# Kernel tuning notes

Measured on AMD Instinct MI355X. Metric: run time of the kernel, lower is better.

Reference implementation:

```python
import jax, jax.numpy as jnp
import numpy as np

STDS = np.array([0.1, 0.1, 0.2, 0.2], np.float32)
MEANS = np.array([0.0, 0.0, 0.0, 0.0], np.float32)
NMS_THRESH = 0.3  # cfg.TEST.NMS


def _decode_clip(boxes, deltas, iminfo):
    # boxes [R,4] (x1,y1,x2,y2), deltas [R,C,4] (unnormalized), iminfo [3]=(h,w,scale)
    w = boxes[:, 2] - boxes[:, 0] + 1.0
    h = boxes[:, 3] - boxes[:, 1] + 1.0
    cx = boxes[:, 0] + 0.5 * w
    cy = boxes[:, 1] + 0.5 * h
    pcx = deltas[..., 0] * w[:, None] + cx[:, None]
    pcy = deltas[..., 1] * h[:, None] + cy[:, None]
    pw = jnp.exp(deltas[..., 2]) * w[:, None]
    ph = jnp.exp(deltas[..., 3]) * h[:, None]
    x1 = pcx - 0.5 * pw
    y1 = pcy - 0.5 * ph
    x2 = pcx + 0.5 * pw
    y2 = pcy + 0.5 * ph
    x1 = jnp.clip(x1, 0.0, iminfo[1] - 1.0)
    x2 = jnp.clip(x2, 0.0, iminfo[1] - 1.0)
    y1 = jnp.clip(y1, 0.0, iminfo[0] - 1.0)
    y2 = jnp.clip(y2, 0.0, iminfo[0] - 1.0)
    return jnp.stack([x1, y1, x2, y2], axis=-1)  # [R,C,4]


def _nms_keep(boxes, valid):
    # boxes [R,4] sorted by score desc; valid [R] bool. Greedy hard NMS, fixed shape.
    b = jax.lax.stop_gradient(boxes)
    R = b.shape[0]
    x1, y1, x2, y2 = b[:, 0], b[:, 1], b[:, 2], b[:, 3]
    area = jnp.maximum(x2 - x1, 0.0) * jnp.maximum(y2 - y1, 0.0)
    xx1 = jnp.maximum(x1[:, None], x1[None, :])
    yy1 = jnp.maximum(y1[:, None], y1[None, :])
    xx2 = jnp.minimum(x2[:, None], x2[None, :])
    yy2 = jnp.minimum(y2[:, None], y2[None, :])
    inter = jnp.maximum(xx2 - xx1, 0.0) * jnp.maximum(yy2 - yy1, 0.0)
    iou = inter / (area[:, None] + area[None, :] - inter + 1e-9)
    ar = jnp.arange(R)
    def body(i, keep):
        sup = (iou[i] > NMS_THRESH) & (ar > i) & keep[i]
        return keep & ~sup
    return jax.lax.fori_loop(0, R, body, valid)


def _per_class(scores, boxes, thresh, cls_id):
    # scores [R], boxes [R,4], scalar thresh, scalar class id
    valid = scores > thresh
    s = jnp.where(valid, scores, -jnp.inf)
    order = jnp.argsort(-s)
    b = boxes[order]
    v = valid[order]
    keep = _nms_keep(b, v)
    dets = jnp.concatenate([b, jnp.full((b.shape[0], 1), cls_id, b.dtype)], axis=1)  # [R,5]
    return dets, keep


def _per_image(scores, pred_boxes, thr, num_pad):
    # scores [R,C], pred_boxes [R,C,4], thr [C]
    C = scores.shape[1]
    cls_ids = jnp.arange(1, C, dtype=scores.dtype)
    dets, keep = jax.vmap(_per_class, in_axes=(1, 1, 0, 0))(
        scores[:, 1:], pred_boxes[:, 1:], thr[1:], cls_ids)  # [C-1,R,5], [C-1,R]
    dets = dets.reshape(-1, 5)   # class-major order == torch.cat over classes
    keep = keep.reshape(-1)
    pos = jnp.cumsum(keep) - 1
    write = keep & (pos < num_pad)  # truncate to num_pad like the original
    idx = jnp.where(write, pos, num_pad)  # overflow bucket
    out = jnp.zeros((num_pad + 1, 5), dets.dtype).at[idx].add(
        dets * write[:, None].astype(dets.dtype))
    n = jnp.minimum(keep.sum(), num_pad)
    return out[:num_pad], n  # zero-padded [num_pad,5], count


def reference(cls_prob, rois, bbox_pred, im_info, per_class_threshold, num_classes):
    B, R, C = cls_prob.shape
    deltas = bbox_pred.reshape(B, R, C, 4) * STDS + MEANS
    pred = jax.vmap(_decode_clip)(rois[:, :, 1:5], deltas, im_info)  # [B,R,C,4]
    gt, n = jax.vmap(lambda s, p: _per_image(s, p, per_class_threshold, num_classes))(
        cls_prob, pred)
    return gt, n


def setup_inputs() -> dict:
    key = jax.random.key(0)
    B, R, C = 2, 1000, 81
    ks = jax.random.split(key, 6)
    cls_prob = jax.nn.softmax(2.0 * jax.random.normal(ks[0], (B, R, C)), axis=-1)
    cx = jax.random.uniform(ks[1], (B, R)) * 1200.0 + 50.0
    cy = jax.random.uniform(ks[2], (B, R)) * 700.0 + 50.0
    bw = jax.random.uniform(ks[3], (B, R)) * 300.0 + 16.0
    bh = jax.random.uniform(ks[4], (B, R)) * 300.0 + 16.0
    x1 = jnp.clip(cx - 0.5 * bw, 0.0, 1332.0)
    x2 = jnp.clip(cx + 0.5 * bw, 0.0, 1332.0)
    y1 = jnp.clip(cy - 0.5 * bh, 0.0, 799.0)
    y2 = jnp.clip(cy + 0.5 * bh, 0.0, 799.0)
    rois = jnp.concatenate([jnp.zeros((B, R, 1)), jnp.stack([x1, y1, x2, y2], -1)], -1)
    bbox_pred = 0.5 * jax.random.normal(ks[5], (B, R, 4 * C))
    im_info = jnp.tile(jnp.array([[800.0, 1333.0, 1.0]], jnp.float32), (B, 1))
    per_class_threshold = jnp.full((C,), 0.05, jnp.float32)
    return {"cls_prob": cls_prob, "rois": rois, "bbox_pred": bbox_pred,
            "im_info": im_info, "per_class_threshold": per_class_threshold,
            "num_classes": C}
```

## Files before the change

### kernel.cpp

```cpp
#include <hip/hip_runtime.h>
#include <math.h>

#define MAXC 1024
#define NMS_T 0.3f

__global__ __launch_bounds__(256) void nms_class_kernel(
    const float* __restrict__ cls_prob, const float* __restrict__ rois,
    const float* __restrict__ bbox_pred, const float* __restrict__ im_info,
    const float* __restrict__ thr, float* __restrict__ ws_boxes,
    int* __restrict__ ws_counts, int B, int R, int C)
{
    const int task = blockIdx.x;
    const int NC = C - 1;
    const int b = task / NC;
    const int c = 1 + (task % NC);
    const int tid = threadIdx.x;

    __shared__ int s_cnt;
    __shared__ float s_sc[MAXC];
    __shared__ int   s_ri[MAXC];
    __shared__ float s_bx[MAXC][4];
    __shared__ float s_area[MAXC];
    __shared__ int   s_keep[MAXC];

    if (tid == 0) s_cnt = 0;
    __syncthreads();

    const float tc = thr[c];
    for (int r = tid; r < R; r += blockDim.x) {
        float s = cls_prob[((size_t)b * R + r) * C + c];
        if (s > tc) {
            int p = atomicAdd(&s_cnt, 1);
            if (p < MAXC) { s_sc[p] = s; s_ri[p] = r; }
        }
    }
    __syncthreads();
    int K = s_cnt; if (K > MAXC) K = MAXC;

    const float maxx = im_info[b * 3 + 1] - 1.0f;
    const float maxy = im_info[b * 3 + 0] - 1.0f;

    for (int i = tid; i < K; i += blockDim.x) {
        const float si = s_sc[i];
        const int   ri = s_ri[i];
        int rank = 0;
        for (int j = 0; j < K; j++) {
            float sj = s_sc[j];
            rank += (sj > si) || (sj == si && s_ri[j] < ri);
        }
        const float* rp = rois + ((size_t)b * R + ri) * 5;
        float rx1 = rp[1], ry1 = rp[2], rx2 = rp[3], ry2 = rp[4];
        float w  = rx2 - rx1 + 1.0f;
        float h  = ry2 - ry1 + 1.0f;
        float cx = rx1 + 0.5f * w;
        float cy = ry1 + 0.5f * h;
        const float* dp = bbox_pred + (((size_t)b * R + ri) * C + c) * 4;
        float d0 = dp[0] * 0.1f, d1 = dp[1] * 0.1f;
        float d2 = dp[2] * 0.2f, d3 = dp[3] * 0.2f;
        float pcx = d0 * w + cx;
        float pcy = d1 * h + cy;
        float pw  = expf(d2) * w;
        float ph  = expf(d3) * h;
        float x1 = fminf(fmaxf(pcx - 0.5f * pw, 0.0f), maxx);
        float x2 = fminf(fmaxf(pcx + 0.5f * pw, 0.0f), maxx);
        float y1 = fminf(fmaxf(pcy - 0.5f * ph, 0.0f), maxy);
        float y2 = fminf(fmaxf(pcy + 0.5f * ph, 0.0f), maxy);
        s_bx[rank][0] = x1; s_bx[rank][1] = y1;
        s_bx[rank][2] = x2; s_bx[rank][3] = y2;
        s_area[rank] = fmaxf(x2 - x1, 0.0f) * fmaxf(y2 - y1, 0.0f);
        s_keep[rank] = 1;
    }
    __syncthreads();

    for (int i = 0; i < K; i++) {
        __syncthreads();
        if (s_keep[i]) {
            float bx1 = s_bx[i][0], by1 = s_bx[i][1];
            float bx2 = s_bx[i][2], by2 = s_bx[i][3];
            float ai  = s_area[i];
            for (int j = i + 1 + tid; j < K; j += blockDim.x) {
                if (s_keep[j]) {
                    float xx1 = fmaxf(bx1, s_bx[j][0]);
                    float yy1 = fmaxf(by1, s_bx[j][1]);
                    float xx2 = fminf(bx2, s_bx[j][2]);
                    float yy2 = fminf(by2, s_bx[j][3]);
                    float inter = fmaxf(xx2 - xx1, 0.0f) * fmaxf(yy2 - yy1, 0.0f);
                    float iou = inter / (ai + s_area[j] - inter + 1e-9f);
                    if (iou > NMS_T) s_keep[j] = 0;
                }
            }
        }
    }
    __syncthreads();

    if (tid == 0) {
        float* dst = ws_boxes + (size_t)task * C * 5;
        int kept = 0;
        float cid = (float)c;
        for (int i = 0; i < K; i++) {
            if (s_keep[i]) {
                if (kept < C) {
                    dst[kept * 5 + 0] = s_bx[i][0];
                    dst[kept * 5 + 1] = s_bx[i][1];
                    dst[kept * 5 + 2] = s_bx[i][2];
                    dst[kept * 5 + 3] = s_bx[i][3];
                    dst[kept * 5 + 4] = cid;
                }
                kept++;
            }
        }
        ws_counts[task] = kept;
    }
}

__global__ __launch_bounds__(256) void pack_kernel(
    const float* __restrict__ ws_boxes, const int* __restrict__ ws_counts,
    float* __restrict__ gt, float* __restrict__ nout, int B, int C)
{
    const int b = blockIdx.x;
    const int tid = threadIdx.x;
    const int NC = C - 1;
    const int P = C;
    __shared__ int s_off[256];
    __shared__ int s_total;

    if (tid == 0) {
        int acc = 0;
        for (int c = 0; c < NC; c++) { s_off[c] = acc; acc += ws_counts[b * NC + c]; }
        s_total = acc;
    }
    __syncthreads();
    const int n = (s_total < P) ? s_total : P;

    for (int i = tid; i < P * 5; i += blockDim.x)
        gt[(size_t)b * P * 5 + i] = 0.0f;
    __syncthreads();

    for (int idx = tid; idx < NC * P; idx += blockDim.x) {
        int c = idx / P, k = idx % P;
        int cnt = ws_counts[b * NC + c]; if (cnt > P) cnt = P;
        if (k < cnt) {
            int pos = s_off[c] + k;
            if (pos < P) {
                const float* src = ws_boxes + (((size_t)(b * NC + c)) * P + k) * 5;
                float* d = gt + ((size_t)b * P + pos) * 5;
                d[0] = src[0]; d[1] = src[1]; d[2] = src[2]; d[3] = src[3]; d[4] = src[4];
            }
        }
    }
    if (tid == 0) nout[b] = (float)n;
}

extern "C" void kernel_launch(void* const* d_in, const int* in_sizes, int n_in,
                              void* d_out, int out_size, void* d_ws, size_t ws_size,
                              hipStream_t stream) {
    const float* cls_prob  = (const float*)d_in[0];
    const float* rois      = (const float*)d_in[1];
    const float* bbox_pred = (const float*)d_in[2];
    const float* im_info   = (const float*)d_in[3];
    const float* thr       = (const float*)d_in[4];

    const int B = in_sizes[3] / 3;
    const int C = in_sizes[4];
    const int R = in_sizes[0] / (B * C);
    const int NC = C - 1;

    float* ws_boxes = (float*)d_ws;
    int*   ws_counts = (int*)(ws_boxes + (size_t)B * NC * C * 5);

    float* gt   = (float*)d_out;
    float* nout = (float*)d_out + (size_t)B * C * 5;

    nms_class_kernel<<<B * NC, 256, 0, stream>>>(
        cls_prob, rois, bbox_pred, im_info, thr, ws_boxes, ws_counts, B, R, C);
    pack_kernel<<<B, 256, 0, stream>>>(ws_boxes, ws_counts, gt, nout, B, C);
}
```

Baseline: 100.5 us.

## Run per-class NMS in a single wavefront with ballot-based compaction and register keep masks

Shrinks the NMS block to one 64-lane wavefront. Candidate compaction now uses ballot and popcount instead of shared atomics. When there are at most 256 candidates, greedy suppression runs on register-resident boxes with 64-bit keep masks updated by ballot, which removes the per-iteration __syncthreads. Kept boxes are written in parallel instead of by a single thread. The pack kernel also computes its prefix offsets in parallel from cached counts. The trade-off is fewer threads per block for the rank and decode phase, plus a slower fallback path when there are more than 256 candidates.

```diff
diff --git a/kernel.cpp b/kernel.cpp
--- a/kernel.cpp
+++ b/kernel.cpp
@@ -4,7 +4,7 @@
 #define MAXC 1024
 #define NMS_T 0.3f
 
-__global__ __launch_bounds__(256) void nms_class_kernel(
+__global__ __launch_bounds__(64) void nms_class_kernel(
     const float* __restrict__ cls_prob, const float* __restrict__ rois,
     const float* __restrict__ bbox_pred, const float* __restrict__ im_info,
     const float* __restrict__ thr, float* __restrict__ ws_boxes,
@@ -15,38 +15,48 @@
     const int b = task / NC;
     const int c = 1 + (task % NC);
     const int tid = threadIdx.x;
-
-    __shared__ int s_cnt;
-    __shared__ float s_sc[MAXC];
-    __shared__ int   s_ri[MAXC];
-    __shared__ float s_bx[MAXC][4];
-    __shared__ float s_area[MAXC];
-    __shared__ int   s_keep[MAXC];
-
-    if (tid == 0) s_cnt = 0;
-    __syncthreads();
+    const unsigned long long lane_lt = (1ull << tid) - 1ull;
+
+    __shared__ float  s_sc[MAXC];
+    __shared__ int    s_ri[MAXC];
+    __shared__ float4 s_bx[MAXC];
+    __shared__ float  s_area[MAXC];
+    __shared__ int    s_keep[MAXC];
 
     const float tc = thr[c];
-    for (int r = tid; r < R; r += blockDim.x) {
-        float s = cls_prob[((size_t)b * R + r) * C + c];
-        if (s > tc) {
-            int p = atomicAdd(&s_cnt, 1);
-            if (p < MAXC) { s_sc[p] = s; s_ri[p] = r; }
-        }
-    }
-    __syncthreads();
-    int K = s_cnt; if (K > MAXC) K = MAXC;
+    int base = 0;
+    for (int r0 = 0; r0 < R; r0 += 64 * 16) {
+        float v[16];
+#pragma unroll
+        for (int k = 0; k < 16; k++) {
+            int r = r0 + k * 64 + tid;
+            v[k] = (r < R) ? cls_prob[((size_t)b * R + r) * C + c] : -1.0f;
+        }
+#pragma unroll
+        for (int k = 0; k < 16; k++) {
+            int r = r0 + k * 64 + tid;
+            bool valid = v[k] > tc;
+            unsigned long long m = __ballot(valid);
+            if (valid) {
+                int pos = base + __popcll(m & lane_lt);
+                if (pos < MAXC) { s_sc[pos] = v[k]; s_ri[pos] = r; }
+            }
+            base += __popcll(m);
+        }
+    }
+    int K = (base < MAXC) ? base : MAXC;
+    __syncthreads();
 
     const float maxx = im_info[b * 3 + 1] - 1.0f;
     const float maxy = im_info[b * 3 + 0] - 1.0f;
 
-    for (int i = tid; i < K; i += blockDim.x) {
-        const float si = s_sc[i];
-        const int   ri = s_ri[i];
+    for (int cand = tid; cand < K; cand += 64) {
+        const float si = s_sc[cand];
+        const int   ri = s_ri[cand];
         int rank = 0;
         for (int j = 0; j < K; j++) {
-            float sj = s_sc[j];
-            rank += (sj > si) || (sj == si && s_ri[j] < ri);
+            float sj = s_sc[j]; int rj = s_ri[j];
+            rank += (sj > si) || (sj == si && rj < ri);
         }
         const float* rp = rois + ((size_t)b * R + ri) * 5;
         float rx1 = rp[1], ry1 = rp[2], rx2 = rp[3], ry2 = rp[4];
@@ -65,51 +75,107 @@
         float x2 = fminf(fmaxf(pcx + 0.5f * pw, 0.0f), maxx);
         float y1 = fminf(fmaxf(pcy - 0.5f * ph, 0.0f), maxy);
         float y2 = fminf(fmaxf(pcy + 0.5f * ph, 0.0f), maxy);
-        s_bx[rank][0] = x1; s_bx[rank][1] = y1;
-        s_bx[rank][2] = x2; s_bx[rank][3] = y2;
+        s_bx[rank] = make_float4(x1, y1, x2, y2);
         s_area[rank] = fmaxf(x2 - x1, 0.0f) * fmaxf(y2 - y1, 0.0f);
-        s_keep[rank] = 1;
-    }
-    __syncthreads();
-
-    for (int i = 0; i < K; i++) {
+    }
+    __syncthreads();
+
+    float* dst = ws_boxes + (size_t)task * C * 5;
+    const float cid = (float)c;
+    const int nchunk = (K + 63) >> 6;
+
+    if (nchunk <= 4) {
+        float jx1[4], jy1[4], jx2[4], jy2[4], jar[4];
+        unsigned long long km[4];
+#pragma unroll
+        for (int q = 0; q < 4; q++) {
+            int idx = q * 64 + tid;
+            float4 bj = (idx < K) ? s_bx[idx] : make_float4(0.f, 0.f, 0.f, 0.f);
+            jx1[q] = bj.x; jy1[q] = bj.y; jx2[q] = bj.z; jy2[q] = bj.w;
+            jar[q] = (idx < K) ? s_area[idx] : 0.0f;
+            int rem = K - q * 64;
+            km[q] = (rem >= 64) ? ~0ull : ((rem > 0) ? ((1ull << rem) - 1ull) : 0ull);
+        }
+        for (int i = 0; i < K; i++) {
+            int ci = i >> 6, li = i & 63;
+            unsigned long long kw = (ci == 0) ? km[0] : (ci == 1) ? km[1]
+                                   : (ci == 2) ? km[2] : km[3];
+            if ((kw >> li) & 1ull) {
+                float4 bi = s_bx[i];
+                float ai = s_area[i];
+#pragma unroll
+                for (int q = 0; q < 4; q++) {
+                    int j = q * 64 + tid;
+                    float xx1 = fmaxf(bi.x, jx1[q]);
+                    float yy1 = fmaxf(bi.y, jy1[q]);
+                    float xx2 = fminf(bi.z, jx2[q]);
+                    float yy2 = fminf(bi.w, jy2[q]);
+                    float inter = fmaxf(xx2 - xx1, 0.0f) * fmaxf(yy2 - yy1, 0.0f);
+                    float iou = inter / (ai + jar[q] - inter + 1e-9f);
+                    bool sup = (j < K) && (j > i) && (iou > NMS_T);
+                    km[q] &= ~__ballot(sup);
+                }
+            }
+        }
+        int pc[4];
+#pragma unroll
+        for (int q = 0; q < 4; q++) pc[q] = __popcll(km[q]);
+        int total = pc[0] + pc[1] + pc[2] + pc[3];
+        int chunk_base = 0;
+#pragma unroll
+        for (int q = 0; q < 4; q++) {
+            int j = q * 64 + tid;
+            if (j < K && ((km[q] >> tid) & 1ull)) {
+                int pos = chunk_base + __popcll(km[q] & lane_lt);
+                if (pos < C) {
+                    dst[pos * 5 + 0] = jx1[q];
+                    dst[pos * 5 + 1] = jy1[q];
+                    dst[pos * 5 + 2] = jx2[q];
+                    dst[pos * 5 + 3] = jy2[q];
+                    dst[pos * 5 + 4] = cid;
+                }
+            }
+            chunk_base += pc[q];
+        }
+        if (tid == 0) ws_counts[task] = total;
+    } else {
+        for (int i = tid; i < K; i += 64) s_keep[i] = 1;
         __syncthreads();
-        if (s_keep[i]) {
-            float bx1 = s_bx[i][0], by1 = s_bx[i][1];
-            float bx2 = s_bx[i][2], by2 = s_bx[i][3];
-            float ai  = s_area[i];
-            for (int j = i + 1 + tid; j < K; j += blockDim.x) {
-                if (s_keep[j]) {
-                    float xx1 = fmaxf(bx1, s_bx[j][0]);
-                    float yy1 = fmaxf(by1, s_bx[j][1]);
-                    float xx2 = fminf(bx2, s_bx[j][2]);
-                    float yy2 = fminf(by2, s_bx[j][3]);
-                    float inter = fmaxf(xx2 - xx1, 0.0f) * fmaxf(yy2 - yy1, 0.0f);
-                    float iou = inter / (ai + s_area[j] - inter + 1e-9f);
-                    if (iou > NMS_T) s_keep[j] = 0;
-                }
-            }
-        }
-    }
-    __syncthreads();
-
-    if (tid == 0) {
-        float* dst = ws_boxes + (size_t)task * C * 5;
-        int kept = 0;
-        float cid = (float)c;
         for (int i = 0; i < K; i++) {
             if (s_keep[i]) {
-                if (kept < C) {
-                    dst[kept * 5 + 0] = s_bx[i][0];
-                    dst[kept * 5 + 1] = s_bx[i][1];
-                    dst[kept * 5 + 2] = s_bx[i][2];
-                    dst[kept * 5 + 3] = s_bx[i][3];
-                    dst[kept * 5 + 4] = cid;
-                }
-                kept++;
-            }
-        }
-        ws_counts[task] = kept;
+                float4 bi = s_bx[i];
+                float ai = s_area[i];
+                for (int j = i + 1 + tid; j < K; j += 64) {
+                    if (s_keep[j]) {
+                        float xx1 = fmaxf(bi.x, s_bx[j].x);
+                        float yy1 = fmaxf(bi.y, s_bx[j].y);
+                        float xx2 = fminf(bi.z, s_bx[j].z);
+                        float yy2 = fminf(bi.w, s_bx[j].w);
+                        float inter = fmaxf(xx2 - xx1, 0.0f) * fmaxf(yy2 - yy1, 0.0f);
+                        float iou = inter / (ai + s_area[j] - inter + 1e-9f);
+                        if (iou > NMS_T) s_keep[j] = 0;
+                    }
+                }
+            }
+            __syncthreads();
+        }
+        if (tid == 0) {
+            int kept = 0;
+            for (int i = 0; i < K; i++) {
+                if (s_keep[i]) {
+                    if (kept < C) {
+                        float4 bv = s_bx[i];
+                        dst[kept * 5 + 0] = bv.x;
+                        dst[kept * 5 + 1] = bv.y;
+                        dst[kept * 5 + 2] = bv.z;
+                        dst[kept * 5 + 3] = bv.w;
+                        dst[kept * 5 + 4] = cid;
+                    }
+                    kept++;
+                }
+            }
+            ws_counts[task] = kept;
+        }
     }
 }
 
@@ -121,13 +187,20 @@
     const int tid = threadIdx.x;
     const int NC = C - 1;
     const int P = C;
+    __shared__ int s_cnt[256];
     __shared__ int s_off[256];
     __shared__ int s_total;
 
-    if (tid == 0) {
+    if (tid < NC) s_cnt[tid] = ws_counts[b * NC + tid];
+    __syncthreads();
+    if (tid < NC) {
         int acc = 0;
-        for (int c = 0; c < NC; c++) { s_off[c] = acc; acc += ws_counts[b * NC + c]; }
-        s_total = acc;
+        for (int cc = 0; cc < NC; cc++) {
+            int v = s_cnt[cc];
+            if (cc < tid) acc += v;
+        }
+        s_off[tid] = acc;
+        if (tid == NC - 1) s_total = acc + s_cnt[tid];
     }
     __syncthreads();
     const int n = (s_total < P) ? s_total : P;
@@ -137,8 +210,8 @@
     __syncthreads();
 
     for (int idx = tid; idx < NC * P; idx += blockDim.x) {
-        int c = idx / P, k = idx % P;
-        int cnt = ws_counts[b * NC + c]; if (cnt > P) cnt = P;
+        int c = idx / P, k = idx - c * P;
+        int cnt = s_cnt[c]; if (cnt > P) cnt = P;
         if (k < cnt) {
             int pos = s_off[c] + k;
             if (pos < P) {
@@ -171,7 +244,7 @@
     float* gt   = (float*)d_out;
     float* nout = (float*)d_out + (size_t)B * C * 5;
 
-    nms_class_kernel<<<B * NC, 256, 0, stream>>>(
+    nms_class_kernel<<<B * NC, 64, 0, stream>>>(
         cls_prob, rois, bbox_pred, im_info, thr, ws_boxes, ws_counts, B, R, C);
     pack_kernel<<<B, 256, 0, stream>>>(ws_boxes, ws_counts, gt, nout, B, C);
 }
```

New measurement: 99.24 us. About the same (-1.2%).
